# Performance work log

Measured on AMD Instinct MI355X. Metric: run time of the kernel, lower is better.

## Reference

```python
import jax, jax.numpy as jnp
import numpy as np
from jax import lax

NO_STEPS = 32


def make_identity_grid(D, H, W, dtype=jnp.float32):
    # matches learnsim init_identity_grid_3d: [1, D, H, W, 3] with last dim (x, y, z)
    xs = jnp.linspace(-1.0, 1.0, W, dtype=dtype)
    ys = jnp.linspace(-1.0, 1.0, H, dtype=dtype)
    zs = jnp.linspace(-1.0, 1.0, D, dtype=dtype)
    gz, gy, gx = jnp.meshgrid(zs, ys, xs, indexing='ij')  # each [D, H, W]
    return jnp.stack([gx, gy, gz], axis=-1)[None]  # [1, D, H, W, 3]


def grid_sample_3d(vol, grid):
    # vol: [N, C, D, H, W]; grid: [N, D, H, W, 3] normalized (x,y,z)
    # trilinear, padding_mode='border', align_corners=True
    N, C, D, H, W = vol.shape
    ix = jnp.clip((grid[..., 0] + 1.0) * 0.5 * (W - 1), 0.0, W - 1)
    iy = jnp.clip((grid[..., 1] + 1.0) * 0.5 * (H - 1), 0.0, H - 1)
    iz = jnp.clip((grid[..., 2] + 1.0) * 0.5 * (D - 1), 0.0, D - 1)
    x0f, y0f, z0f = jnp.floor(ix), jnp.floor(iy), jnp.floor(iz)
    fx, fy, fz = ix - x0f, iy - y0f, iz - z0f  # fractional weights [N,D,H,W]
    x0 = x0f.astype(jnp.int32); y0 = y0f.astype(jnp.int32); z0 = z0f.astype(jnp.int32)
    x1 = jnp.minimum(x0 + 1, W - 1)
    y1 = jnp.minimum(y0 + 1, H - 1)
    z1 = jnp.minimum(z0 + 1, D - 1)

    def sample_one(vol_b, z0b, z1b, y0b, y1b, x0b, x1b, fxb, fyb, fzb):
        vflat = vol_b.reshape(C, -1)  # [C, D*H*W]
        def g(zi, yi, xi):
            idx = (zi * H + yi) * W + xi
            return jnp.take(vflat, idx.reshape(-1), axis=1).reshape(C, D, H, W)
        wx0, wy0, wz0 = 1.0 - fxb, 1.0 - fyb, 1.0 - fzb
        out = (g(z0b, y0b, x0b) * (wz0 * wy0 * wx0)
             + g(z0b, y0b, x1b) * (wz0 * wy0 * fxb)
             + g(z0b, y1b, x0b) * (wz0 * fyb * wx0)
             + g(z0b, y1b, x1b) * (wz0 * fyb * fxb)
             + g(z1b, y0b, x0b) * (fzb * wy0 * wx0)
             + g(z1b, y0b, x1b) * (fzb * wy0 * fxb)
             + g(z1b, y1b, x0b) * (fzb * fyb * wx0)
             + g(z1b, y1b, x1b) * (fzb * fyb * fxb))
        return out

    return jax.vmap(sample_one)(vol, z0, z1, y0, y1, x0, x1, fx, fy, fz)


def setup_inputs() -> dict:
    key = jax.random.key(0)
    N, C, D, H, W = 2, 3, 128, 128, 128
    v = jax.random.normal(key, (N, C, D, H, W), dtype=jnp.float32)
    identity_grid = make_identity_grid(D, H, W)
    return {"v": v, "identity_grid": identity_grid}


def reference(v, identity_grid):
    # scaling-and-squaring integration of a stationary velocity field
    N = v.shape[0]
    disp0 = v / jnp.asarray(2.0 ** NO_STEPS, v.dtype)

    def step(disp, _):
        # [N, D, H, W, 3] warp grid
        transformation = identity_grid + jnp.transpose(disp, (0, 2, 3, 4, 1))
        disp = disp + grid_sample_3d(disp, transformation)
        return disp, None

    displacement, _ = lax.scan(step, disp0, None, length=NO_STEPS)
    transformation = jnp.transpose(identity_grid, (0, 4, 1, 2, 3)) + displacement
    return (transformation, displacement)
```

## Files before the change

kernel.cpp:

```cpp
#include <hip/hip_runtime.h>


#define NSTEPS 32

constexpr int Dd = 128, Hh = 128, Ww = 128, Nb = 2, Cc = 3;
constexpr int VOX = Dd * Hh * Ww;
constexpr int NV  = Nb * VOX;
constexpr int THREADS = 256;
constexpr int NBLK = NV / THREADS;
constexpr int NXCD = 8;

__device__ float g_tab[3 * 128];

__global__ __launch_bounds__(128) void extract_tables(const float* __restrict__ idg) {
    int t = threadIdx.x;
    g_tab[t]       = idg[3 * t];
    g_tab[128 + t] = idg[3 * (t << 7) + 1];
    g_tab[256 + t] = idg[3 * (t << 14) + 2];
}

__global__ __launch_bounds__(THREADS) void svf_init(const float* __restrict__ v,
                                                    float4* __restrict__ A) {
    int i = blockIdx.x * THREADS + threadIdx.x;
    int n = i >> 21;
    int s = i & (VOX - 1);
    const float sc = 2.3283064365386963e-10f;
    int b = n * Cc * VOX + s;
    float dx = v[b]           * sc;
    float dy = v[b + VOX]     * sc;
    float dz = v[b + 2 * VOX] * sc;
    A[i] = make_float4(dx, dy, dz, 0.0f);
}

__global__ __launch_bounds__(THREADS) void svf_step(const float4* __restrict__ src,
                                                    float4* __restrict__ dst) {
    int bid = blockIdx.x;
    int swz = (bid & (NXCD - 1)) * (NBLK / NXCD) + (bid >> 3);
    int i = swz * THREADS + threadIdx.x;
    int s = i & (VOX - 1);
    int base = i - s;

    int xg = s & 127;
    int yg = (s >> 7) & 127;
    int zg = s >> 14;

    float4 d = src[i];
    float id_x = g_tab[xg];
    float id_y = g_tab[128 + yg];
    float id_z = g_tab[256 + zg];

    float ix = ((id_x + d.x) + 1.0f) * 0.5f * 127.0f;
    float iy = ((id_y + d.y) + 1.0f) * 0.5f * 127.0f;
    float iz = ((id_z + d.z) + 1.0f) * 0.5f * 127.0f;
    ix = fminf(fmaxf(ix, 0.0f), 127.0f);
    iy = fminf(fmaxf(iy, 0.0f), 127.0f);
    iz = fminf(fmaxf(iz, 0.0f), 127.0f);

    float x0f = floorf(ix), y0f = floorf(iy), z0f = floorf(iz);
    float fx = ix - x0f, fy = iy - y0f, fz = iz - z0f;
    int x0 = (int)x0f, y0 = (int)y0f, z0 = (int)z0f;
    int x1 = min(x0 + 1, 127);
    int y1 = min(y0 + 1, 127);
    int z1 = min(z0 + 1, 127);

    float wx0 = 1.0f - fx, wy0 = 1.0f - fy, wz0 = 1.0f - fz;

    int r00 = base + (z0 << 14) + (y0 << 7);
    int r01 = base + (z0 << 14) + (y1 << 7);
    int r10 = base + (z1 << 14) + (y0 << 7);
    int r11 = base + (z1 << 14) + (y1 << 7);

    float4 g000 = src[r00 + x0];
    float4 g001 = src[r00 + x1];
    float4 g010 = src[r01 + x0];
    float4 g011 = src[r01 + x1];
    float4 g100 = src[r10 + x0];
    float4 g101 = src[r10 + x1];
    float4 g110 = src[r11 + x0];
    float4 g111 = src[r11 + x1];

    float w000 = wz0 * wy0 * wx0;
    float w001 = wz0 * wy0 * fx;
    float w010 = wz0 * fy  * wx0;
    float w011 = wz0 * fy  * fx;
    float w100 = fz  * wy0 * wx0;
    float w101 = fz  * wy0 * fx;
    float w110 = fz  * fy  * wx0;
    float w111 = fz  * fy  * fx;

    float ox = g000.x * w000 + g001.x * w001 + g010.x * w010 + g011.x * w011
             + g100.x * w100 + g101.x * w101 + g110.x * w110 + g111.x * w111;
    float oy = g000.y * w000 + g001.y * w001 + g010.y * w010 + g011.y * w011
             + g100.y * w100 + g101.y * w101 + g110.y * w110 + g111.y * w111;
    float oz = g000.z * w000 + g001.z * w001 + g010.z * w010 + g011.z * w011
             + g100.z * w100 + g101.z * w101 + g110.z * w110 + g111.z * w111;

    dst[i] = make_float4(d.x + ox, d.y + oy, d.z + oz, 0.0f);
}

__global__ __launch_bounds__(THREADS) void svf_final(const float4* __restrict__ A,
                                                     float* __restrict__ out) {
    int i = blockIdx.x * THREADS + threadIdx.x;
    int n = i >> 21;
    int s = i & (VOX - 1);

    int xg = s & 127;
    int yg = (s >> 7) & 127;
    int zg = s >> 14;

    float4 d = A[i];
    float id_x = g_tab[xg];
    float id_y = g_tab[128 + yg];
    float id_z = g_tab[256 + zg];

    int ob = n * Cc * VOX + s;
    out[ob]            = id_x + d.x;
    out[ob + VOX]      = id_y + d.y;
    out[ob + 2 * VOX]  = id_z + d.z;
    float* disp_out = out + (size_t)Nb * Cc * VOX;
    disp_out[ob]           = d.x;
    disp_out[ob + VOX]     = d.y;
    disp_out[ob + 2 * VOX] = d.z;
}

extern "C" void kernel_launch(void* const* d_in, const int* in_sizes, int n_in,
                              void* d_out, int out_size, void* d_ws, size_t ws_size,
                              hipStream_t stream) {
    const float* v   = (const float*)d_in[0];
    const float* idg = (const float*)d_in[1];
    float* out = (float*)d_out;

    float4* A = (float4*)d_ws;
    float4* B = (float4*)d_out;

    dim3 grid(NBLK), block(THREADS);

    extract_tables<<<1, 128, 0, stream>>>(idg);
    svf_init<<<grid, block, 0, stream>>>(v, A);
    for (int k = 0; k < NSTEPS; ++k) {
        const float4* src = (k & 1) ? (const float4*)B : (const float4*)A;
        float4*       dst = (k & 1) ? A : B;
        svf_step<<<grid, block, 0, stream>>>(src, dst);
    }
    svf_final<<<grid, block, 0, stream>>>(A, out);
}
```

Measured before the change: 1.388 ms.

## Stage neighborhood tiles in LDS for early steps and fuse init/final into steps

Early scaling-and-squaring steps have tiny displacements, so the first 26 steps use a tiled kernel. It loads an 8x12x12 halo block (for an 8x8x4 output tile) into shared memory and gathers the trilinear corners from LDS, falling back to global loads when a corner lies outside the tile. The init conversion is fused into the first step and the final output write into the last step, which removes two full passes over the volume. This costs redundant halo loads, a block-wide sync and more LDS per block. The K_TILED threshold is a heuristic for when displacements grow beyond the 2-voxel halo.

```diff
diff --git a/kernel.cpp b/kernel.cpp
--- a/kernel.cpp
+++ b/kernel.cpp
@@ -3,12 +3,12 @@
 
 #define NSTEPS 32
 
-constexpr int Dd = 128, Hh = 128, Ww = 128, Nb = 2, Cc = 3;
-constexpr int VOX = Dd * Hh * Ww;
-constexpr int NV  = Nb * VOX;
+constexpr int VOX = 1 << 21;
+constexpr int NV  = 2 * VOX;
 constexpr int THREADS = 256;
 constexpr int NBLK = NV / THREADS;
 constexpr int NXCD = 8;
+constexpr int K_TILED = 26;
 
 __device__ float g_tab[3 * 128];
 
@@ -19,66 +19,11 @@
     g_tab[256 + t] = idg[3 * (t << 14) + 2];
 }
 
-__global__ __launch_bounds__(THREADS) void svf_init(const float* __restrict__ v,
-                                                    float4* __restrict__ A) {
-    int i = blockIdx.x * THREADS + threadIdx.x;
-    int n = i >> 21;
-    int s = i & (VOX - 1);
-    const float sc = 2.3283064365386963e-10f;
-    int b = n * Cc * VOX + s;
-    float dx = v[b]           * sc;
-    float dy = v[b + VOX]     * sc;
-    float dz = v[b + 2 * VOX] * sc;
-    A[i] = make_float4(dx, dy, dz, 0.0f);
-}
-
-__global__ __launch_bounds__(THREADS) void svf_step(const float4* __restrict__ src,
-                                                    float4* __restrict__ dst) {
-    int bid = blockIdx.x;
-    int swz = (bid & (NXCD - 1)) * (NBLK / NXCD) + (bid >> 3);
-    int i = swz * THREADS + threadIdx.x;
-    int s = i & (VOX - 1);
-    int base = i - s;
-
-    int xg = s & 127;
-    int yg = (s >> 7) & 127;
-    int zg = s >> 14;
-
-    float4 d = src[i];
-    float id_x = g_tab[xg];
-    float id_y = g_tab[128 + yg];
-    float id_z = g_tab[256 + zg];
-
-    float ix = ((id_x + d.x) + 1.0f) * 0.5f * 127.0f;
-    float iy = ((id_y + d.y) + 1.0f) * 0.5f * 127.0f;
-    float iz = ((id_z + d.z) + 1.0f) * 0.5f * 127.0f;
-    ix = fminf(fmaxf(ix, 0.0f), 127.0f);
-    iy = fminf(fmaxf(iy, 0.0f), 127.0f);
-    iz = fminf(fmaxf(iz, 0.0f), 127.0f);
-
-    float x0f = floorf(ix), y0f = floorf(iy), z0f = floorf(iz);
-    float fx = ix - x0f, fy = iy - y0f, fz = iz - z0f;
-    int x0 = (int)x0f, y0 = (int)y0f, z0 = (int)z0f;
-    int x1 = min(x0 + 1, 127);
-    int y1 = min(y0 + 1, 127);
-    int z1 = min(z0 + 1, 127);
-
+__device__ __forceinline__ float4 trilerp_accum(
+    float4 d, float4 g000, float4 g001, float4 g010, float4 g011,
+    float4 g100, float4 g101, float4 g110, float4 g111,
+    float fx, float fy, float fz) {
     float wx0 = 1.0f - fx, wy0 = 1.0f - fy, wz0 = 1.0f - fz;
-
-    int r00 = base + (z0 << 14) + (y0 << 7);
-    int r01 = base + (z0 << 14) + (y1 << 7);
-    int r10 = base + (z1 << 14) + (y0 << 7);
-    int r11 = base + (z1 << 14) + (y1 << 7);
-
-    float4 g000 = src[r00 + x0];
-    float4 g001 = src[r00 + x1];
-    float4 g010 = src[r01 + x0];
-    float4 g011 = src[r01 + x1];
-    float4 g100 = src[r10 + x0];
-    float4 g101 = src[r10 + x1];
-    float4 g110 = src[r11 + x0];
-    float4 g111 = src[r11 + x1];
-
     float w000 = wz0 * wy0 * wx0;
     float w001 = wz0 * wy0 * fx;
     float w010 = wz0 * fy  * wx0;
@@ -87,40 +32,195 @@
     float w101 = fz  * wy0 * fx;
     float w110 = fz  * fy  * wx0;
     float w111 = fz  * fy  * fx;
-
     float ox = g000.x * w000 + g001.x * w001 + g010.x * w010 + g011.x * w011
              + g100.x * w100 + g101.x * w101 + g110.x * w110 + g111.x * w111;
     float oy = g000.y * w000 + g001.y * w001 + g010.y * w010 + g011.y * w011
              + g100.y * w100 + g101.y * w101 + g110.y * w110 + g111.y * w111;
     float oz = g000.z * w000 + g001.z * w001 + g010.z * w010 + g011.z * w011
              + g100.z * w100 + g101.z * w101 + g110.z * w110 + g111.z * w111;
-
-    dst[i] = make_float4(d.x + ox, d.y + oy, d.z + oz, 0.0f);
-}
-
-__global__ __launch_bounds__(THREADS) void svf_final(const float4* __restrict__ A,
-                                                     float* __restrict__ out) {
-    int i = blockIdx.x * THREADS + threadIdx.x;
+    return make_float4(d.x + ox, d.y + oy, d.z + oz, 0.0f);
+}
+
+template<bool FIRST>
+__global__ __launch_bounds__(THREADS, 4) void svf_step_tiled(
+        const float4* __restrict__ src, const float* __restrict__ v,
+        float4* __restrict__ dst) {
+    __shared__ float4 tile[8][12][13];
+
+    int bid = blockIdx.x;
+    int swz = (bid & (NXCD - 1)) * (NBLK / NXCD) + (bid >> 3);
+    int n = swz >> 13;
+    int t = swz & 8191;
+    int bx0 = (t & 15) << 3;
+    int by0 = ((t >> 4) & 15) << 3;
+    int bz0 = (t >> 8) << 2;
+
+    const int nbase  = n << 21;
+    const int nbase3 = 3 * nbase;
+    const float sc = 2.3283064365386963e-10f;
+
+    int tid = threadIdx.x;
+    for (int idx = tid; idx < 8 * 12 * 12; idx += THREADS) {
+        int lx = idx % 12;
+        int r  = idx / 12;
+        int ly = r % 12;
+        int lz = r / 12;
+        int gx = min(max(bx0 + lx - 2, 0), 127);
+        int gy = min(max(by0 + ly - 2, 0), 127);
+        int gz = min(max(bz0 + lz - 2, 0), 127);
+        int s = (gz << 14) + (gy << 7) + gx;
+        float4 val;
+        if (FIRST) {
+            int b = nbase3 + s;
+            val = make_float4(v[b] * sc, v[b + VOX] * sc, v[b + 2 * VOX] * sc, 0.0f);
+        } else {
+            val = src[nbase + s];
+        }
+        tile[lz][ly][lx] = val;
+    }
+    __syncthreads();
+
+    int tx = tid & 7, ty = (tid >> 3) & 7, tz = tid >> 6;
+    int gx = bx0 + tx, gy = by0 + ty, gz = bz0 + tz;
+    int s = (gz << 14) + (gy << 7) + gx;
+
+    float4 d = tile[tz + 2][ty + 2][tx + 2];
+    float id_x = g_tab[gx];
+    float id_y = g_tab[128 + gy];
+    float id_z = g_tab[256 + gz];
+
+    float ix = ((id_x + d.x) + 1.0f) * 0.5f * 127.0f;
+    float iy = ((id_y + d.y) + 1.0f) * 0.5f * 127.0f;
+    float iz = ((id_z + d.z) + 1.0f) * 0.5f * 127.0f;
+    ix = fminf(fmaxf(ix, 0.0f), 127.0f);
+    iy = fminf(fmaxf(iy, 0.0f), 127.0f);
+    iz = fminf(fmaxf(iz, 0.0f), 127.0f);
+
+    float x0f = floorf(ix), y0f = floorf(iy), z0f = floorf(iz);
+    float fx = ix - x0f, fy = iy - y0f, fz = iz - z0f;
+    int x0 = (int)x0f, y0 = (int)y0f, z0 = (int)z0f;
+    int x1 = min(x0 + 1, 127);
+    int y1 = min(y0 + 1, 127);
+    int z1 = min(z0 + 1, 127);
+
+    int lx0 = x0 - bx0 + 2, lx1 = x1 - bx0 + 2;
+    int ly0 = y0 - by0 + 2, ly1 = y1 - by0 + 2;
+    int lz0 = z0 - bz0 + 2, lz1 = z1 - bz0 + 2;
+    bool inT = (unsigned)lx0 < 12u && (unsigned)lx1 < 12u
+            && (unsigned)ly0 < 12u && (unsigned)ly1 < 12u
+            && (unsigned)lz0 < 8u  && (unsigned)lz1 < 8u;
+
+    float4 g000, g001, g010, g011, g100, g101, g110, g111;
+    if (inT) {
+        g000 = tile[lz0][ly0][lx0];
+        g001 = tile[lz0][ly0][lx1];
+        g010 = tile[lz0][ly1][lx0];
+        g011 = tile[lz0][ly1][lx1];
+        g100 = tile[lz1][ly0][lx0];
+        g101 = tile[lz1][ly0][lx1];
+        g110 = tile[lz1][ly1][lx0];
+        g111 = tile[lz1][ly1][lx1];
+    } else {
+        int r00 = (z0 << 14) + (y0 << 7);
+        int r01 = (z0 << 14) + (y1 << 7);
+        int r10 = (z1 << 14) + (y0 << 7);
+        int r11 = (z1 << 14) + (y1 << 7);
+        if (FIRST) {
+            auto ldv = [&](int ss) {
+                int b = nbase3 + ss;
+                return make_float4(v[b] * sc, v[b + VOX] * sc, v[b + 2 * VOX] * sc, 0.0f);
+            };
+            g000 = ldv(r00 + x0); g001 = ldv(r00 + x1);
+            g010 = ldv(r01 + x0); g011 = ldv(r01 + x1);
+            g100 = ldv(r10 + x0); g101 = ldv(r10 + x1);
+            g110 = ldv(r11 + x0); g111 = ldv(r11 + x1);
+        } else {
+            g000 = src[nbase + r00 + x0]; g001 = src[nbase + r00 + x1];
+            g010 = src[nbase + r01 + x0]; g011 = src[nbase + r01 + x1];
+            g100 = src[nbase + r10 + x0]; g101 = src[nbase + r10 + x1];
+            g110 = src[nbase + r11 + x0]; g111 = src[nbase + r11 + x1];
+        }
+    }
+
+    dst[nbase + s] = trilerp_accum(d, g000, g001, g010, g011,
+                                   g100, g101, g110, g111, fx, fy, fz);
+}
+
+__global__ __launch_bounds__(THREADS) void svf_step(const float4* __restrict__ src,
+                                                    float4* __restrict__ dst) {
+    int bid = blockIdx.x;
+    int swz = (bid & (NXCD - 1)) * (NBLK / NXCD) + (bid >> 3);
+    int i = swz * THREADS + threadIdx.x;
+    int s = i & (VOX - 1);
+    int base = i - s;
+
+    int xg = s & 127, yg = (s >> 7) & 127, zg = s >> 14;
+
+    float4 d = src[i];
+    float ix = ((g_tab[xg] + d.x) + 1.0f) * 0.5f * 127.0f;
+    float iy = ((g_tab[128 + yg] + d.y) + 1.0f) * 0.5f * 127.0f;
+    float iz = ((g_tab[256 + zg] + d.z) + 1.0f) * 0.5f * 127.0f;
+    ix = fminf(fmaxf(ix, 0.0f), 127.0f);
+    iy = fminf(fmaxf(iy, 0.0f), 127.0f);
+    iz = fminf(fmaxf(iz, 0.0f), 127.0f);
+
+    float x0f = floorf(ix), y0f = floorf(iy), z0f = floorf(iz);
+    float fx = ix - x0f, fy = iy - y0f, fz = iz - z0f;
+    int x0 = (int)x0f, y0 = (int)y0f, z0 = (int)z0f;
+    int x1 = min(x0 + 1, 127), y1 = min(y0 + 1, 127), z1 = min(z0 + 1, 127);
+
+    int r00 = base + (z0 << 14) + (y0 << 7);
+    int r01 = base + (z0 << 14) + (y1 << 7);
+    int r10 = base + (z1 << 14) + (y0 << 7);
+    int r11 = base + (z1 << 14) + (y1 << 7);
+
+    dst[i] = trilerp_accum(d, src[r00 + x0], src[r00 + x1], src[r01 + x0], src[r01 + x1],
+                           src[r10 + x0], src[r10 + x1], src[r11 + x0], src[r11 + x1],
+                           fx, fy, fz);
+}
+
+__global__ __launch_bounds__(THREADS) void svf_step_last(const float4* __restrict__ src,
+                                                         float* __restrict__ out) {
+    int bid = blockIdx.x;
+    int swz = (bid & (NXCD - 1)) * (NBLK / NXCD) + (bid >> 3);
+    int i = swz * THREADS + threadIdx.x;
+    int s = i & (VOX - 1);
+    int base = i - s;
     int n = i >> 21;
-    int s = i & (VOX - 1);
-
-    int xg = s & 127;
-    int yg = (s >> 7) & 127;
-    int zg = s >> 14;
-
-    float4 d = A[i];
-    float id_x = g_tab[xg];
-    float id_y = g_tab[128 + yg];
-    float id_z = g_tab[256 + zg];
-
-    int ob = n * Cc * VOX + s;
-    out[ob]            = id_x + d.x;
-    out[ob + VOX]      = id_y + d.y;
-    out[ob + 2 * VOX]  = id_z + d.z;
-    float* disp_out = out + (size_t)Nb * Cc * VOX;
-    disp_out[ob]           = d.x;
-    disp_out[ob + VOX]     = d.y;
-    disp_out[ob + 2 * VOX] = d.z;
+
+    int xg = s & 127, yg = (s >> 7) & 127, zg = s >> 14;
+    float id_x = g_tab[xg], id_y = g_tab[128 + yg], id_z = g_tab[256 + zg];
+
+    float4 d = src[i];
+    float ix = ((id_x + d.x) + 1.0f) * 0.5f * 127.0f;
+    float iy = ((id_y + d.y) + 1.0f) * 0.5f * 127.0f;
+    float iz = ((id_z + d.z) + 1.0f) * 0.5f * 127.0f;
+    ix = fminf(fmaxf(ix, 0.0f), 127.0f);
+    iy = fminf(fmaxf(iy, 0.0f), 127.0f);
+    iz = fminf(fmaxf(iz, 0.0f), 127.0f);
+
+    float x0f = floorf(ix), y0f = floorf(iy), z0f = floorf(iz);
+    float fx = ix - x0f, fy = iy - y0f, fz = iz - z0f;
+    int x0 = (int)x0f, y0 = (int)y0f, z0 = (int)z0f;
+    int x1 = min(x0 + 1, 127), y1 = min(y0 + 1, 127), z1 = min(z0 + 1, 127);
+
+    int r00 = base + (z0 << 14) + (y0 << 7);
+    int r01 = base + (z0 << 14) + (y1 << 7);
+    int r10 = base + (z1 << 14) + (y0 << 7);
+    int r11 = base + (z1 << 14) + (y1 << 7);
+
+    float4 nd = trilerp_accum(d, src[r00 + x0], src[r00 + x1], src[r01 + x0], src[r01 + x1],
+                              src[r10 + x0], src[r10 + x1], src[r11 + x0], src[r11 + x1],
+                              fx, fy, fz);
+
+    int ob = n * 3 * VOX + s;
+    out[ob]           = id_x + nd.x;
+    out[ob + VOX]     = id_y + nd.y;
+    out[ob + 2 * VOX] = id_z + nd.z;
+    float* dout = out + (size_t)2 * 3 * VOX;
+    dout[ob]           = nd.x;
+    dout[ob + VOX]     = nd.y;
+    dout[ob + 2 * VOX] = nd.z;
 }
 
 extern "C" void kernel_launch(void* const* d_in, const int* in_sizes, int n_in,
@@ -136,11 +236,16 @@
     dim3 grid(NBLK), block(THREADS);
 
     extract_tables<<<1, 128, 0, stream>>>(idg);
-    svf_init<<<grid, block, 0, stream>>>(v, A);
-    for (int k = 0; k < NSTEPS; ++k) {
-        const float4* src = (k & 1) ? (const float4*)B : (const float4*)A;
-        float4*       dst = (k & 1) ? A : B;
-        svf_step<<<grid, block, 0, stream>>>(src, dst);
-    }
-    svf_final<<<grid, block, 0, stream>>>(A, out);
-}
+    svf_step_tiled<true><<<grid, block, 0, stream>>>(nullptr, v, A);
+    for (int k = 1; k < K_TILED; ++k) {
+        const float4* srck = (k & 1) ? (const float4*)A : (const float4*)B;
+        float4*       dstk = (k & 1) ? B : A;
+        svf_step_tiled<false><<<grid, block, 0, stream>>>(srck, nullptr, dstk);
+    }
+    for (int k = K_TILED; k < NSTEPS - 1; ++k) {
+        const float4* srck = (k & 1) ? (const float4*)A : (const float4*)B;
+        float4*       dstk = (k & 1) ? B : A;
+        svf_step<<<grid, block, 0, stream>>>(srck, dstk);
+    }
+    svf_step_last<<<grid, block, 0, stream>>>((const float4*)A, out);
+}
```

Result: slower. 1.599 ms (+15.2%).
